# Performance work log

Hardware: AMD Instinct MI355X
Metric: run time of the kernel (lower is better)

Reference implementation:

```python
import jax, jax.numpy as jnp
import numpy as np

DIM = 1024
HEADS = 16
DIM_HEAD = 64
INNER = HEADS * DIM_HEAD
EPS = 1e-6


def elu_feature_map(t):
    # F.elu(x) + 1
    return jnp.where(t > 0, t + 1.0, jnp.exp(t))


def setup_inputs() -> dict:
    key = jax.random.key(0)
    k1, k2, k3, k4 = jax.random.split(key, 4)
    B, N = 4, 8192
    x = jax.random.normal(k1, (B, N, DIM), dtype=jnp.float32)
    s_in = 1.0 / np.sqrt(DIM)
    s_out = 1.0 / np.sqrt(INNER)
    Wqkv = jax.random.uniform(k2, (DIM, 3 * INNER), dtype=jnp.float32, minval=-s_in, maxval=s_in)
    Wout = jax.random.uniform(k3, (INNER, DIM), dtype=jnp.float32, minval=-s_out, maxval=s_out)
    bout = jax.random.uniform(k4, (DIM,), dtype=jnp.float32, minval=-s_out, maxval=s_out)
    return {"x": x, "Wqkv": Wqkv, "Wout": Wout, "bout": bout}


def reference(x, Wqkv, Wout, bout):
    B, N, D = x.shape
    qkv = x @ Wqkv  # [B,N,3*INNER]
    q, k, v = jnp.split(qkv, 3, axis=-1)
    # b n (h d) -> b h n d
    resh = lambda t: t.reshape(B, N, HEADS, DIM_HEAD).transpose(0, 2, 1, 3)
    q, k, v = resh(q), resh(k), resh(v)
    q = elu_feature_map(q)
    k = elu_feature_map(k)
    kv = jnp.einsum('bhnd,bhnf->bhdf', k, v)          # [B,H,d,d]
    k_sum = k.sum(axis=-2)                             # [B,H,d]
    qkv_out = jnp.einsum('bhnd,bhdf->bhnf', q, kv)    # [B,H,N,d]
    q_k_sum = jnp.einsum('bhnd,bhd->bhn', q, k_sum)   # [B,H,N]
    out = qkv_out / (q_k_sum[..., None] + EPS)
    out = out.transpose(0, 2, 1, 3).reshape(B, N, INNER)  # b h n d -> b n (h d)
    return out @ Wout + bout
```

## Files before the change

### kernel.cpp

```cpp
#include <hip/hip_runtime.h>
#include <hip/hip_bf16.h>
#include <math.h>


typedef unsigned short ushort_t;
typedef __attribute__((ext_vector_type(8))) short s8v;
typedef __attribute__((ext_vector_type(4))) float f32x4;

#define MFMA(a,b,c) __builtin_amdgcn_mfma_f32_16x16x32_bf16((a),(b),(c),0,0,0)

typedef __attribute__((address_space(3))) unsigned int as3_u32;
typedef __attribute__((address_space(1))) const unsigned int as1_u32c;

__device__ __forceinline__ void g2l16(const void* g, void* l) {
    __builtin_amdgcn_global_load_lds((as1_u32c*)g, (as3_u32*)l, 16, 0, 0);
}

__device__ __forceinline__ float bf2f(ushort_t u) {
    union { float f; unsigned v; } x; x.v = ((unsigned)u) << 16; return x.f;
}
__device__ __forceinline__ ushort_t f2bf(float f) {
    union { float f; unsigned v; } x; x.f = f;
    unsigned r = x.v + 0x7fffu + ((x.v >> 16) & 1u);
    return (ushort_t)(r >> 16);
}
__device__ __forceinline__ float elu1(float t) { return t > 0.0f ? t + 1.0f : expf(t); }

__global__ void k_cast(const float* __restrict__ in, ushort_t* __restrict__ out, int n8) {
    int i = blockIdx.x * blockDim.x + threadIdx.x;
    if (i >= n8) return;
    const float4* p = (const float4*)in;
    float4 a = p[(size_t)i * 2], b = p[(size_t)i * 2 + 1];
    uint4 o;
    o.x = (unsigned)f2bf(a.x) | ((unsigned)f2bf(a.y) << 16);
    o.y = (unsigned)f2bf(a.z) | ((unsigned)f2bf(a.w) << 16);
    o.z = (unsigned)f2bf(b.x) | ((unsigned)f2bf(b.y) << 16);
    o.w = (unsigned)f2bf(b.z) | ((unsigned)f2bf(b.w) << 16);
    *(uint4*)(out + (size_t)i * 8) = o;
}

__global__ __launch_bounds__(256) void k_transpose(const float* __restrict__ W,
                                                   ushort_t* __restrict__ WT, int K, int N) {
    __shared__ float s[32][33];
    const int t = threadIdx.x;
    const int k0 = blockIdx.x * 32, n0 = blockIdx.y * 32;
    const int kr = t >> 3, n4 = (t & 7) * 4;
    float4 v = *(const float4*)(W + (size_t)(k0 + kr) * N + n0 + n4);
    s[kr][n4 + 0] = v.x; s[kr][n4 + 1] = v.y; s[kr][n4 + 2] = v.z; s[kr][n4 + 3] = v.w;
    __syncthreads();
    const int nr = kr, k4 = n4;
    unsigned lo = (unsigned)f2bf(s[k4 + 0][nr]) | ((unsigned)f2bf(s[k4 + 1][nr]) << 16);
    unsigned hi = (unsigned)f2bf(s[k4 + 2][nr]) | ((unsigned)f2bf(s[k4 + 3][nr]) << 16);
    *(uint2*)(WT + (size_t)(n0 + nr) * K + k0 + k4) = make_uint2(lo, hi);
}

template<int MODE, int NFR>
__global__ __launch_bounds__(512, 2) void k_gemm(
    const ushort_t* __restrict__ A, const ushort_t* __restrict__ B,
    ushort_t* __restrict__ obf, const float* __restrict__ bout, float* __restrict__ of)
{
    constexpr int BN   = NFR * 64;
    constexpr int ASZ  = 256 * 64;
    constexpr int BSZ  = BN * 64;
    constexpr int BUFS = ASZ + BSZ;
    constexpr int BCHW = NFR;
    __shared__ ushort_t lds[2 * BUFS];

    const int t = threadIdx.x, l = t & 63, w = t >> 6;
    const int wr = w >> 2, wc = w & 3;
    const size_t m0 = (size_t)blockIdx.x * 256;
    const size_t n0 = (size_t)blockIdx.y * BN;

    f32x4 acc[8][NFR];
    const f32x4 z = {0.f, 0.f, 0.f, 0.f};
#pragma unroll
    for (int i = 0; i < 8; i++)
#pragma unroll
        for (int j = 0; j < NFR; j++) acc[i][j] = z;

    const int lr  = l >> 3;
    const int lco = ((l & 7) ^ lr) << 3;
    const ushort_t* gA = A + (m0 + (size_t)(32 * w) + lr) * 1024 + lco;
    const ushort_t* gB = B + (n0 + (size_t)(8 * BCHW * w) + lr) * 1024 + lco;
    const int la15 = l & 15;
    const int exo  = (((l >> 4) ^ (l & 7)) << 3);

#pragma unroll
    for (int i = 0; i < 4; i++)
        g2l16(gA + (size_t)(8 * i) * 1024, &lds[(w * 4 + i) * 512]);
#pragma unroll
    for (int i = 0; i < BCHW; i++)
        g2l16(gB + (size_t)(8 * i) * 1024, &lds[ASZ + (w * BCHW + i) * 512]);
    asm volatile("s_waitcnt vmcnt(0)" ::: "memory");
    __builtin_amdgcn_sched_barrier(0);
    __builtin_amdgcn_s_barrier();
    __builtin_amdgcn_sched_barrier(0);

    for (int T = 0; T < 16; ++T) {
        const int base  = (T & 1) * BUFS;
        const int nbase = BUFS - base;
        const bool st   = (T < 15);
        const size_t k1 = (size_t)(T + 1) * 64;
        s8v af[4], bf[NFR];

        if (st) {
#pragma unroll
            for (int i = 0; i < 4; i++)
                g2l16(gA + (size_t)(8 * i) * 1024 + k1, &lds[nbase + (w * 4 + i) * 512]);
        }
#pragma unroll
        for (int nf = 0; nf < NFR; nf++)
            bf[nf] = *(const s8v*)&lds[base + ASZ + (wc * (16 * NFR) + nf * 16 + la15) * 64 + exo];
#pragma unroll
        for (int i = 0; i < 4; i++)
            af[i] = *(const s8v*)&lds[base + (wr * 128 + i * 16 + la15) * 64 + exo];
        __builtin_amdgcn_s_setprio(1);
#pragma unroll
        for (int i = 0; i < 4; i++)
#pragma unroll
            for (int nf = 0; nf < NFR; nf++)
                acc[i][nf] = MFMA(af[i], bf[nf], acc[i][nf]);
        __builtin_amdgcn_s_setprio(0);
        __builtin_amdgcn_s_barrier();
        __builtin_amdgcn_sched_barrier(0);

        if (st) {
#pragma unroll
            for (int i = 0; i < BCHW; i++)
                g2l16(gB + (size_t)(8 * i) * 1024 + k1, &lds[nbase + ASZ + (w * BCHW + i) * 512]);
        }
#pragma unroll
        for (int i = 0; i < 4; i++)
            af[i] = *(const s8v*)&lds[base + (wr * 128 + 64 + i * 16 + la15) * 64 + exo];
        __builtin_amdgcn_s_setprio(1);
#pragma unroll
        for (int i = 0; i < 4; i++)
#pragma unroll
            for (int nf = 0; nf < NFR; nf++)
                acc[4 + i][nf] = MFMA(af[i], bf[nf], acc[4 + i][nf]);
        __builtin_amdgcn_s_setprio(0);
        __builtin_amdgcn_s_barrier();
        __builtin_amdgcn_sched_barrier(0);

#pragma unroll
        for (int nf = 0; nf < NFR; nf++)
            bf[nf] = *(const s8v*)&lds[base + ASZ + (wc * (16 * NFR) + nf * 16 + la15) * 64 + (32 ^ exo)];
#pragma unroll
        for (int i = 0; i < 4; i++)
            af[i] = *(const s8v*)&lds[base + (wr * 128 + i * 16 + la15) * 64 + (32 ^ exo)];
        __builtin_amdgcn_s_setprio(1);
#pragma unroll
        for (int i = 0; i < 4; i++)
#pragma unroll
            for (int nf = 0; nf < NFR; nf++)
                acc[i][nf] = MFMA(af[i], bf[nf], acc[i][nf]);
        __builtin_amdgcn_s_setprio(0);
        __builtin_amdgcn_s_barrier();
        __builtin_amdgcn_sched_barrier(0);

#pragma unroll
        for (int i = 0; i < 4; i++)
            af[i] = *(const s8v*)&lds[base + (wr * 128 + 64 + i * 16 + la15) * 64 + (32 ^ exo)];
        __builtin_amdgcn_s_setprio(1);
#pragma unroll
        for (int i = 0; i < 4; i++)
#pragma unroll
            for (int nf = 0; nf < NFR; nf++)
                acc[4 + i][nf] = MFMA(af[i], bf[nf], acc[4 + i][nf]);
        __builtin_amdgcn_s_setprio(0);
        __builtin_amdgcn_sched_barrier(0);
        if (st) asm volatile("s_waitcnt vmcnt(0)" ::: "memory");
        __builtin_amdgcn_sched_barrier(0);
        __builtin_amdgcn_s_barrier();
        __builtin_amdgcn_sched_barrier(0);
    }

    const int r4 = (l >> 4) * 4;
    if (MODE == 0) {
#pragma unroll
        for (int mf = 0; mf < 8; mf++)
#pragma unroll
            for (int nf = 0; nf < NFR; nf++) {
                const size_t colb = n0 + wc * (16 * NFR) + nf * 16;
                const bool feat = colb < 2048;
#pragma unroll
                for (int r = 0; r < 4; r++) {
                    const size_t row = m0 + wr * 128 + mf * 16 + r4 + r;
                    float v = acc[mf][nf][r];
                    obf[row * 3072 + colb + la15] = f2bf(feat ? elu1(v) : v);
                }
            }
    } else {
#pragma unroll
        for (int mf = 0; mf < 8; mf++)
#pragma unroll
            for (int nf = 0; nf < NFR; nf++) {
                const size_t col = n0 + wc * (16 * NFR) + nf * 16 + la15;
                const float bo = bout[col];
#pragma unroll
                for (int r = 0; r < 4; r++) {
                    const size_t row = m0 + wr * 128 + mf * 16 + r4 + r;
                    of[row * 1024 + col] = acc[mf][nf][r] + bo;
                }
            }
    }
}

#define KST 136
__global__ __launch_bounds__(256) void k_kv(
    const ushort_t* __restrict__ qkv, float* __restrict__ kv, float* __restrict__ ksum)
{
    __shared__ ushort_t kT[64 * KST];
    __shared__ ushort_t vT[64 * KST];
    __shared__ float ksl[64];
    const int t = threadIdx.x, l = t & 63, w = t >> 6;
    const int wr = w >> 1, wc = w & 1;
    const int h = blockIdx.x;
    const int b = blockIdx.z;
    const ushort_t* qkvb = qkv + (size_t)b * 8192 * 3072;
    float* kvh = kv + ((size_t)b * 16 + h) * 4096;
    float* ksh = ksum + (size_t)b * 1024 + h * 64;
    const int n00 = blockIdx.y * 512;
    const f32x4 z = {0.f, 0.f, 0.f, 0.f};
    f32x4 acc[2][2] = {{z, z}, {z, z}};
    float ksloc[4] = {0.f, 0.f, 0.f, 0.f};
    const int sd0 = (t & 15) * 4;
    if (t < 64) ksl[t] = 0.f;

    for (int c = 0; c < 4; c++) {
        __syncthreads();
        const int n0 = n00 + c * 128;
#pragma unroll
        for (int i = 0; i < 8; i++) {
            int n = i * 16 + (t >> 4);
            const ushort_t* kp = qkvb + (size_t)(n0 + n) * 3072 + 1024 + h * 64 + sd0;
            ushort4 kw = *(const ushort4*)kp;
            ushort4 vw = *(const ushort4*)(kp + 1024);
            ksloc[0] += bf2f(kw.x); ksloc[1] += bf2f(kw.y);
            ksloc[2] += bf2f(kw.z); ksloc[3] += bf2f(kw.w);
            kT[(sd0 + 0) * KST + n] = kw.x; kT[(sd0 + 1) * KST + n] = kw.y;
            kT[(sd0 + 2) * KST + n] = kw.z; kT[(sd0 + 3) * KST + n] = kw.w;
            vT[(sd0 + 0) * KST + n] = vw.x; vT[(sd0 + 1) * KST + n] = vw.y;
            vT[(sd0 + 2) * KST + n] = vw.z; vT[(sd0 + 3) * KST + n] = vw.w;
        }
        __syncthreads();
#pragma unroll
        for (int kb = 0; kb < 128; kb += 32) {
            s8v af[2], bfr[2];
#pragma unroll
            for (int ma = 0; ma < 2; ma++) {
                int d = wr * 32 + ma * 16 + (l & 15);
                af[ma] = *(const s8v*)&kT[d * KST + kb + (l >> 4) * 8];
            }
#pragma unroll
            for (int fb = 0; fb < 2; fb++) {
                int f = wc * 32 + fb * 16 + (l & 15);
                bfr[fb] = *(const s8v*)&vT[f * KST + kb + (l >> 4) * 8];
            }
#pragma unroll
            for (int ma = 0; ma < 2; ma++)
#pragma unroll
                for (int fb = 0; fb < 2; fb++)
                    acc[ma][fb] = MFMA(af[ma], bfr[fb], acc[ma][fb]);
        }
    }
    atomicAdd(&ksl[sd0 + 0], ksloc[0]); atomicAdd(&ksl[sd0 + 1], ksloc[1]);
    atomicAdd(&ksl[sd0 + 2], ksloc[2]); atomicAdd(&ksl[sd0 + 3], ksloc[3]);
    __syncthreads();
    if (t < 64) atomicAdd(&ksh[t], ksl[t]);
#pragma unroll
    for (int ma = 0; ma < 2; ma++)
#pragma unroll
        for (int fb = 0; fb < 2; fb++)
#pragma unroll
            for (int r = 0; r < 4; r++) {
                int d = wr * 32 + ma * 16 + (l >> 4) * 4 + r;
                int f = wc * 32 + fb * 16 + (l & 15);
                atomicAdd(&kvh[f * 64 + d], acc[ma][fb][r]);
            }
}

#define AST 72
__global__ __launch_bounds__(256) void k_apply(
    const ushort_t* __restrict__ qkv, const float* __restrict__ kv,
    const float* __restrict__ ksum, ushort_t* __restrict__ attn)
{
    __shared__ ushort_t kvb[64 * AST];
    const int t = threadIdx.x, l = t & 63, w = t >> 6;
    const int la15 = l & 15;
    const int row0 = blockIdx.x * 32;
    const int b = row0 >> 13;
    const f32x4 z = {0.f, 0.f, 0.f, 0.f};

    for (int hh = 0; hh < 8; hh++) {
        const int h = blockIdx.y * 8 + hh;
        const float* kvh = kv + ((size_t)b * 16 + h) * 4096;
        const float* ksh = ksum + (size_t)b * 1024 + h * 64;
        __syncthreads();
        {
            const int f = t >> 2, d0 = (t & 3) * 16;
            const float* src = kvh + f * 64 + d0;
            s8v v0, v1;
#pragma unroll
            for (int j = 0; j < 8; j++) {
                v0[j] = (short)f2bf(src[j]);
                v1[j] = (short)f2bf(src[j + 8]);
            }
            *(s8v*)&kvb[f * AST + d0]     = v0;
            *(s8v*)&kvb[f * AST + d0 + 8] = v1;
        }
        __syncthreads();
        float ksv[16];
        {
            const float* kp = ksh + (l >> 4) * 8;
            *(float4*)&ksv[0]  = *(const float4*)(kp);
            *(float4*)&ksv[4]  = *(const float4*)(kp + 4);
            *(float4*)&ksv[8]  = *(const float4*)(kp + 32);
            *(float4*)&ksv[12] = *(const float4*)(kp + 36);
        }
        f32x4 acc[2] = {z, z};
        float pd[2] = {0.f, 0.f};
#pragma unroll
        for (int ks = 0; ks < 2; ks++) {
            const int f = w * 16 + la15;
            s8v bfr = *(const s8v*)&kvb[f * AST + ks * 32 + (l >> 4) * 8];
#pragma unroll
            for (int ma = 0; ma < 2; ma++) {
                int row = row0 + ma * 16 + la15;
                s8v afr = *(const s8v*)(qkv + (size_t)row * 3072 + h * 64 + ks * 32 + (l >> 4) * 8);
#pragma unroll
                for (int j = 0; j < 8; j++)
                    pd[ma] += bf2f((ushort_t)afr[j]) * ksv[ks * 8 + j];
                acc[ma] = MFMA(afr, bfr, acc[ma]);
            }
        }
#pragma unroll
        for (int ma = 0; ma < 2; ma++) {
            pd[ma] += __shfl_xor(pd[ma], 16, 64);
            pd[ma] += __shfl_xor(pd[ma], 32, 64);
        }
#pragma unroll
        for (int ma = 0; ma < 2; ma++)
#pragma unroll
            for (int r = 0; r < 4; r++) {
                int lrow = (l >> 4) * 4 + r;
                float dot = __shfl(pd[ma], lrow, 64);
                float dv = 1.f / (dot + 1e-6f);
                int row = row0 + ma * 16 + lrow;
                int f = w * 16 + la15;
                attn[(size_t)row * 1024 + h * 64 + f] = f2bf(acc[ma][r] * dv);
            }
    }
}

extern "C" void kernel_launch(void* const* d_in, const int* in_sizes, int n_in,
                              void* d_out, int out_size, void* d_ws, size_t ws_size,
                              hipStream_t stream) {
    const float* x    = (const float*)d_in[0];
    const float* Wqkv = (const float*)d_in[1];
    const float* Wout = (const float*)d_in[2];
    const float* bout = (const float*)d_in[3];
    float* out = (float*)d_out;
    char* ws = (char*)d_ws;

    ushort_t* WqkvT = (ushort_t*)(ws + 0);
    ushort_t* WoutT = (ushort_t*)(ws + 6291456);
    float*    kv    = (float*)(ws + 8388608);
    float*    ksum  = (float*)(ws + 12582912);
    ushort_t* xb    = (ushort_t*)(ws + 12599296);
    ushort_t* qkv   = (ushort_t*)(ws + 79708160);
    ushort_t* attn  = (ushort_t*)(ws + 281034752);

    k_transpose<<<dim3(32, 96), 256, 0, stream>>>(Wqkv, WqkvT, 1024, 3072);
    k_transpose<<<dim3(32, 32), 256, 0, stream>>>(Wout, WoutT, 1024, 1024);
    hipMemsetAsync(kv, 0, 4194304 + 16384, stream);
    k_cast<<<16384, 256, 0, stream>>>(x, xb, 4194304);

    k_gemm<0, 3><<<dim3(128, 16), 512, 0, stream>>>(xb, WqkvT, qkv, nullptr, nullptr);
    k_kv<<<dim3(16, 16, 4), 256, 0, stream>>>(qkv, kv, ksum);
    k_apply<<<dim3(1024, 2), 256, 0, stream>>>(qkv, kv, ksum, attn);
    k_gemm<1, 2><<<dim3(128, 8), 512, 0, stream>>>(attn, WoutT, nullptr, bout, out);
}
```

Before: 577.2 us.

## Use 256x256 GEMM tiles and simplify the K-loop pipeline barriers

Both GEMMs now use a fixed 256x256 output tile (8x4 fragments per wave) in place of 256x192 and 256x128 tiles, cutting the grid to 128x12 and 128x4 blocks. Each K step issues all A and B prefetches up front, then runs two half-K MFMA phases with one barrier per iteration instead of four, and skips the final wait on the last iteration. The larger tiles are meant to raise operand reuse and reduce barrier overhead, but they double LDS use to 128KB per block, which likely limits occupancy to one block per CU. They also raise register pressure and leave fewer blocks, especially for the output GEMM.

```diff
diff --git a/kernel.cpp b/kernel.cpp
--- a/kernel.cpp
+++ b/kernel.cpp
@@ -54,34 +54,31 @@
     *(uint2*)(WT + (size_t)(n0 + nr) * K + k0 + k4) = make_uint2(lo, hi);
 }
 
-template<int MODE, int NFR>
+template<int MODE>
 __global__ __launch_bounds__(512, 2) void k_gemm(
     const ushort_t* __restrict__ A, const ushort_t* __restrict__ B,
     ushort_t* __restrict__ obf, const float* __restrict__ bout, float* __restrict__ of)
 {
-    constexpr int BN   = NFR * 64;
     constexpr int ASZ  = 256 * 64;
-    constexpr int BSZ  = BN * 64;
-    constexpr int BUFS = ASZ + BSZ;
-    constexpr int BCHW = NFR;
+    constexpr int BUFS = 2 * ASZ;
     __shared__ ushort_t lds[2 * BUFS];
 
     const int t = threadIdx.x, l = t & 63, w = t >> 6;
     const int wr = w >> 2, wc = w & 3;
     const size_t m0 = (size_t)blockIdx.x * 256;
-    const size_t n0 = (size_t)blockIdx.y * BN;
-
-    f32x4 acc[8][NFR];
+    const size_t n0 = (size_t)blockIdx.y * 256;
+
+    f32x4 acc[8][4];
     const f32x4 z = {0.f, 0.f, 0.f, 0.f};
 #pragma unroll
     for (int i = 0; i < 8; i++)
 #pragma unroll
-        for (int j = 0; j < NFR; j++) acc[i][j] = z;
+        for (int j = 0; j < 4; j++) acc[i][j] = z;
 
     const int lr  = l >> 3;
     const int lco = ((l & 7) ^ lr) << 3;
     const ushort_t* gA = A + (m0 + (size_t)(32 * w) + lr) * 1024 + lco;
-    const ushort_t* gB = B + (n0 + (size_t)(8 * BCHW * w) + lr) * 1024 + lco;
+    const ushort_t* gB = B + (n0 + (size_t)(32 * w) + lr) * 1024 + lco;
     const int la15 = l & 15;
     const int exo  = (((l >> 4) ^ (l & 7)) << 3);
 
@@ -89,8 +86,8 @@
     for (int i = 0; i < 4; i++)
         g2l16(gA + (size_t)(8 * i) * 1024, &lds[(w * 4 + i) * 512]);
 #pragma unroll
-    for (int i = 0; i < BCHW; i++)
-        g2l16(gB + (size_t)(8 * i) * 1024, &lds[ASZ + (w * BCHW + i) * 512]);
+    for (int i = 0; i < 4; i++)
+        g2l16(gB + (size_t)(8 * i) * 1024, &lds[ASZ + (w * 4 + i) * 512]);
     asm volatile("s_waitcnt vmcnt(0)" ::: "memory");
     __builtin_amdgcn_sched_barrier(0);
     __builtin_amdgcn_s_barrier();
@@ -99,80 +96,52 @@
     for (int T = 0; T < 16; ++T) {
         const int base  = (T & 1) * BUFS;
         const int nbase = BUFS - base;
-        const bool st   = (T < 15);
-        const size_t k1 = (size_t)(T + 1) * 64;
-        s8v af[4], bf[NFR];
-
-        if (st) {
+
+        if (T < 15) {
+            const size_t k1 = (size_t)(T + 1) * 64;
 #pragma unroll
             for (int i = 0; i < 4; i++)
                 g2l16(gA + (size_t)(8 * i) * 1024 + k1, &lds[nbase + (w * 4 + i) * 512]);
-        }
-#pragma unroll
-        for (int nf = 0; nf < NFR; nf++)
-            bf[nf] = *(const s8v*)&lds[base + ASZ + (wc * (16 * NFR) + nf * 16 + la15) * 64 + exo];
-#pragma unroll
-        for (int i = 0; i < 4; i++)
-            af[i] = *(const s8v*)&lds[base + (wr * 128 + i * 16 + la15) * 64 + exo];
+#pragma unroll
+            for (int i = 0; i < 4; i++)
+                g2l16(gB + (size_t)(8 * i) * 1024 + k1, &lds[nbase + ASZ + (w * 4 + i) * 512]);
+        }
+
+        s8v af[8], bf[4];
+#pragma unroll
+        for (int nf = 0; nf < 4; nf++)
+            bf[nf] = *(const s8v*)&lds[base + ASZ + (wc * 64 + nf * 16 + la15) * 64 + exo];
+#pragma unroll
+        for (int mf = 0; mf < 8; mf++)
+            af[mf] = *(const s8v*)&lds[base + (wr * 128 + mf * 16 + la15) * 64 + exo];
         __builtin_amdgcn_s_setprio(1);
 #pragma unroll
-        for (int i = 0; i < 4; i++)
-#pragma unroll
-            for (int nf = 0; nf < NFR; nf++)
-                acc[i][nf] = MFMA(af[i], bf[nf], acc[i][nf]);
+        for (int mf = 0; mf < 8; mf++)
+#pragma unroll
+            for (int nf = 0; nf < 4; nf++)
+                acc[mf][nf] = MFMA(af[mf], bf[nf], acc[mf][nf]);
         __builtin_amdgcn_s_setprio(0);
-        __builtin_amdgcn_s_barrier();
-        __builtin_amdgcn_sched_barrier(0);
-
-        if (st) {
-#pragma unroll
-            for (int i = 0; i < BCHW; i++)
-                g2l16(gB + (size_t)(8 * i) * 1024 + k1, &lds[nbase + ASZ + (w * BCHW + i) * 512]);
-        }
-#pragma unroll
-        for (int i = 0; i < 4; i++)
-            af[i] = *(const s8v*)&lds[base + (wr * 128 + 64 + i * 16 + la15) * 64 + exo];
+#pragma unroll
+        for (int nf = 0; nf < 4; nf++)
+            bf[nf] = *(const s8v*)&lds[base + ASZ + (wc * 64 + nf * 16 + la15) * 64 + (32 ^ exo)];
+#pragma unroll
+        for (int mf = 0; mf < 8; mf++)
+            af[mf] = *(const s8v*)&lds[base + (wr * 128 + mf * 16 + la15) * 64 + (32 ^ exo)];
         __builtin_amdgcn_s_setprio(1);
 #pragma unroll
-        for (int i = 0; i < 4; i++)
-#pragma unroll
-            for (int nf = 0; nf < NFR; nf++)
-                acc[4 + i][nf] = MFMA(af[i], bf[nf], acc[4 + i][nf]);
+        for (int mf = 0; mf < 8; mf++)
+#pragma unroll
+            for (int nf = 0; nf < 4; nf++)
+                acc[mf][nf] = MFMA(af[mf], bf[nf], acc[mf][nf]);
         __builtin_amdgcn_s_setprio(0);
-        __builtin_amdgcn_s_barrier();
-        __builtin_amdgcn_sched_barrier(0);
-
-#pragma unroll
-        for (int nf = 0; nf < NFR; nf++)
-            bf[nf] = *(const s8v*)&lds[base + ASZ + (wc * (16 * NFR) + nf * 16 + la15) * 64 + (32 ^ exo)];
-#pragma unroll
-        for (int i = 0; i < 4; i++)
-            af[i] = *(const s8v*)&lds[base + (wr * 128 + i * 16 + la15) * 64 + (32 ^ exo)];
-        __builtin_amdgcn_s_setprio(1);
-#pragma unroll
-        for (int i = 0; i < 4; i++)
-#pragma unroll
-            for (int nf = 0; nf < NFR; nf++)
-                acc[i][nf] = MFMA(af[i], bf[nf], acc[i][nf]);
-        __builtin_amdgcn_s_setprio(0);
-        __builtin_amdgcn_s_barrier();
-        __builtin_amdgcn_sched_barrier(0);
-
-#pragma unroll
-        for (int i = 0; i < 4; i++)
-            af[i] = *(const s8v*)&lds[base + (wr * 128 + 64 + i * 16 + la15) * 64 + (32 ^ exo)];
-        __builtin_amdgcn_s_setprio(1);
-#pragma unroll
-        for (int i = 0; i < 4; i++)
-#pragma unroll
-            for (int nf = 0; nf < NFR; nf++)
-                acc[4 + i][nf] = MFMA(af[i], bf[nf], acc[4 + i][nf]);
-        __builtin_amdgcn_s_setprio(0);
-        __builtin_amdgcn_sched_barrier(0);
-        if (st) asm volatile("s_waitcnt vmcnt(0)" ::: "memory");
-        __builtin_amdgcn_sched_barrier(0);
-        __builtin_amdgcn_s_barrier();
-        __builtin_amdgcn_sched_barrier(0);
+
+        if (T < 15) {
+            __builtin_amdgcn_sched_barrier(0);
+            asm volatile("s_waitcnt vmcnt(0)" ::: "memory");
+            __builtin_amdgcn_sched_barrier(0);
+            __builtin_amdgcn_s_barrier();
+            __builtin_amdgcn_sched_barrier(0);
+        }
     }
 
     const int r4 = (l >> 4) * 4;
@@ -180,8 +149,8 @@
 #pragma unroll
         for (int mf = 0; mf < 8; mf++)
 #pragma unroll
-            for (int nf = 0; nf < NFR; nf++) {
-                const size_t colb = n0 + wc * (16 * NFR) + nf * 16;
+            for (int nf = 0; nf < 4; nf++) {
+                const size_t colb = n0 + wc * 64 + nf * 16;
                 const bool feat = colb < 2048;
 #pragma unroll
                 for (int r = 0; r < 4; r++) {
@@ -194,8 +163,8 @@
 #pragma unroll
         for (int mf = 0; mf < 8; mf++)
 #pragma unroll
-            for (int nf = 0; nf < NFR; nf++) {
-                const size_t col = n0 + wc * (16 * NFR) + nf * 16 + la15;
+            for (int nf = 0; nf < 4; nf++) {
+                const size_t col = n0 + wc * 64 + nf * 16 + la15;
                 const float bo = bout[col];
 #pragma unroll
                 for (int r = 0; r < 4; r++) {
@@ -376,8 +345,8 @@
     hipMemsetAsync(kv, 0, 4194304 + 16384, stream);
     k_cast<<<16384, 256, 0, stream>>>(x, xb, 4194304);
 
-    k_gemm<0, 3><<<dim3(128, 16), 512, 0, stream>>>(xb, WqkvT, qkv, nullptr, nullptr);
+    k_gemm<0><<<dim3(128, 12), 512, 0, stream>>>(xb, WqkvT, qkv, nullptr, nullptr);
     k_kv<<<dim3(16, 16, 4), 256, 0, stream>>>(qkv, kv, ksum);
     k_apply<<<dim3(1024, 2), 256, 0, stream>>>(qkv, kv, ksum, attn);
-    k_gemm<1, 2><<<dim3(128, 8), 512, 0, stream>>>(attn, WoutT, nullptr, bout, out);
-}
+    k_gemm<1><<<dim3(128, 4), 512, 0, stream>>>(attn, WoutT, nullptr, bout, out);
+}
```

After: 518.3 us. -10.2%, faster.
